# Performance work log

Hardware: AMD Instinct MI355X
Metric: run time of the kernel (lower is better)

## Reference

```python
import jax, jax.numpy as jnp
import numpy as np

T = 2048          # tokens
HID = 4096        # hidden_size
H = 32            # n_heads
D = 192           # head_dim
DR = 64           # qk_rope_head_dim
Q_LORA = 1536
O_LORA = 512
G = 4             # o_groups
EPS = 1e-6
MAX_POS = 4096
ROPE_BASE = 10000.0
SCALE = D ** -0.5


def _rmsnorm(x, weight=None, eps=EPS):
    # normalize over last dim in fp32, like the triton kernel / RMSNorm
    xf = x.astype(jnp.float32)
    rms_inv = jax.lax.rsqrt(jnp.mean(xf * xf, axis=-1, keepdims=True) + eps)
    out = xf * rms_inv
    if weight is not None:
        out = out * weight
    return out.astype(x.dtype)


def _apply_rope(x, cos, sin):
    # x: [..., DR]; interleaved complex rotation (deepseek-style freqs_cis mult)
    x2 = x.reshape(x.shape[:-1] + (DR // 2, 2))
    a, b = x2[..., 0], x2[..., 1]
    ra = a * cos - b * sin
    rb = a * sin + b * cos
    return jnp.stack([ra, rb], axis=-1).reshape(x.shape)


def setup_inputs() -> dict:
    key = jax.random.key(0)
    ks = jax.random.split(key, 12)
    s = lambda k, shape, scale: jax.random.normal(k, shape, dtype=jnp.float32) * scale
    x = s(ks[0], (T, HID), 1.0)
    positions = jnp.arange(T, dtype=jnp.int64)
    wq_a = s(ks[1], (Q_LORA, HID), HID ** -0.5)
    q_norm_w = jnp.ones((Q_LORA,), jnp.float32)
    wq_b = s(ks[2], (H * D, Q_LORA), Q_LORA ** -0.5)
    wkv = s(ks[3], (D, HID), HID ** -0.5)
    kv_norm_w = jnp.ones((D,), jnp.float32)
    attn_sink = s(ks[4], (H,), 1.0)
    wo_a = s(ks[5], (G * O_LORA, (H * D) // G), ((H * D) // G) ** -0.5)
    wo_b = s(ks[6], (HID, G * O_LORA), (G * O_LORA) ** -0.5)
    # precomputed rope tables [MAX_POS, DR//2]
    inv_freq = 1.0 / (ROPE_BASE ** (np.arange(0, DR, 2, dtype=np.float32) / DR))
    t = np.arange(MAX_POS, dtype=np.float32)
    freqs = np.outer(t, inv_freq)
    rope_cos = jnp.asarray(np.cos(freqs))
    rope_sin = jnp.asarray(np.sin(freqs))
    return dict(x=x, positions=positions, wq_a=wq_a, q_norm_w=q_norm_w, wq_b=wq_b,
                wkv=wkv, kv_norm_w=kv_norm_w, attn_sink=attn_sink, wo_a=wo_a,
                wo_b=wo_b, rope_cos=rope_cos, rope_sin=rope_sin)


def reference(x, positions, wq_a, q_norm_w, wq_b, wkv, kv_norm_w, attn_sink,
              wo_a, wo_b, rope_cos, rope_sin):
    cos = rope_cos[positions]  # [T, DR//2]
    sin = rope_sin[positions]

    # q path: wq_a -> RMSNorm(weighted) -> wq_b -> per-head unweighted RMSNorm -> RoPE
    q_lora = _rmsnorm(x @ wq_a.T, q_norm_w)                # [T, Q_LORA]
    q = (q_lora @ wq_b.T).reshape(T, H, D)                 # [T, H, D]
    q = _rmsnorm(q)                                        # per-head rms_normalize
    q_rope = _apply_rope(q[..., -DR:], cos[:, None, :], sin[:, None, :])
    q = jnp.concatenate([q[..., :-DR], q_rope], axis=-1)

    # shared single kv head: wkv -> kv_norm -> RoPE on rope dims
    kv = _rmsnorm(x @ wkv.T, kv_norm_w)                    # [T, D]
    kv_rope = _apply_rope(kv[..., -DR:], cos, sin)
    kv = jnp.concatenate([kv[..., :-DR], kv_rope], axis=-1)

    # MQA attention with attention sink and causal mask
    scores = jnp.einsum('thd,sd->ths', q, kv).astype(jnp.float32) * SCALE  # [T,H,S]
    causal = positions[:, None] >= positions[None, :]       # [T, S]
    scores = jnp.where(causal[:, None, :], scores, -jnp.inf)
    sink = jnp.broadcast_to(attn_sink[None, :, None], (T, H, 1))
    logits = jnp.concatenate([scores, sink], axis=-1)       # [T, H, S+1]
    probs = jax.nn.softmax(logits, axis=-1)[..., :-1]       # drop sink column
    out = jnp.einsum('ths,sd->thd', probs.astype(kv.dtype), kv)  # [T, H, D]

    # grouped low-rank output projection: wo_a per group, then wo_b
    out_g = out.reshape(T, G, (H * D) // G)
    wo_a_g = wo_a.reshape(G, O_LORA, (H * D) // G)
    o_low = jnp.einsum('tgi,goi->tgo', out_g, wo_a_g).reshape(T, G * O_LORA)
    y = o_low @ wo_b.T                                      # [T, HID]
    return y
```

## Files before the change

kernel.cpp:

```cpp
#include <hip/hip_runtime.h>
#include <hip/hip_bf16.h>

#define T_TOK 2048
#define HIDN  4096
#define NH    32
#define HD    192
#define QLORA 1536
#define OLORA 512
#define NG    4
#define NFUSE 1728

typedef unsigned short u16;
typedef __attribute__((ext_vector_type(8))) short short8;
typedef __attribute__((ext_vector_type(4))) short short4v;
typedef __attribute__((ext_vector_type(4))) float f32x4;

__device__ __forceinline__ float b2f(u16 u) {
  union { unsigned int u; float f; } x; x.u = ((unsigned int)u) << 16; return x.f;
}
__device__ __forceinline__ u16 f2b(float f) {
  union { float f; unsigned int u; } x; x.f = f;
  unsigned int r = x.u + 0x7fff + ((x.u >> 16) & 1);
  return (u16)(r >> 16);
}

#define GLOAD16(gp, lp) __builtin_amdgcn_global_load_lds( \
    (const __attribute__((address_space(1))) unsigned int*)(gp), \
    (__attribute__((address_space(3))) unsigned int*)(lp), 16, 0, 0)
#define SCHEDB() __builtin_amdgcn_sched_barrier(0)
#define SBAR()   __builtin_amdgcn_s_barrier()

__global__ __launch_bounds__(256) void cast_f32_bf16(const float* __restrict__ src,
                                                     u16* __restrict__ dst, long n4) {
  long i = (long)blockIdx.x * blockDim.x + threadIdx.x;
  long stride = (long)gridDim.x * blockDim.x;
  for (long j = i; j < n4; j += stride) {
    float4 v = *reinterpret_cast<const float4*>(src + j * 4);
    short4v o;
    o[0] = (short)f2b(v.x); o[1] = (short)f2b(v.y);
    o[2] = (short)f2b(v.z); o[3] = (short)f2b(v.w);
    *reinterpret_cast<short4v*>(dst + j * 4) = o;
  }
}

template <int OM>
__global__ __launch_bounds__(256)
void gemm_bt(const u16* __restrict__ A, const u16* __restrict__ B,
             void* __restrict__ Cout, int M, int N, int K,
             int lda, int ldb, int ldc,
             long a_goff, long b_goff, long c_goff) {
  A += (long)blockIdx.z * a_goff;
  B += (long)blockIdx.z * b_goff;
  __shared__ u16 As[2][128 * 32];
  __shared__ u16 Bs[2][128 * 32];
  const int tid = threadIdx.x;
  const int lane = tid & 63;
  const int wave = tid >> 6;
  const int lg = lane >> 4, lr = lane & 15;
  const int wm = (wave >> 1) * 64, wn = (wave & 1) * 64;
  const int m0 = blockIdx.x * 128, n0 = blockIdx.y * 128;

  const int i0 = tid, i1 = tid + 256;
  const int ra0 = i0 >> 2, ka0 = (i0 & 3) * 8;
  const int ra1 = i1 >> 2, ka1 = (i1 & 3) * 8;
  const u16* pA0 = A + (long)(m0 + ra0) * lda + ka0;
  const u16* pA1 = A + (long)(m0 + ra1) * lda + ka1;
  int rb0 = n0 + ra0; if (rb0 > N - 1) rb0 = N - 1;
  int rb1 = n0 + ra1; if (rb1 > N - 1) rb1 = N - 1;
  const u16* pB0 = B + (long)rb0 * ldb + ka0;
  const u16* pB1 = B + (long)rb1 * ldb + ka1;
  const int woff = wave * 1024;

  f32x4 acc[4][4];
#pragma unroll
  for (int a = 0; a < 4; a++)
#pragma unroll
    for (int b = 0; b < 4; b++) acc[a][b] = f32x4{0.f, 0.f, 0.f, 0.f};

  GLOAD16(pA0, (char*)As + woff);
  GLOAD16(pA1, (char*)As + 4096 + woff);
  GLOAD16(pB0, (char*)Bs + woff);
  GLOAD16(pB1, (char*)Bs + 4096 + woff);

  const int nk = K >> 5;
  int buf = 0;
  for (int kk = 0; kk < nk; ++kk) {
    const int kn = (kk + 1 < nk) ? (kk + 1) * 32 : kk * 32;
    {
      char* dA = (char*)As + (buf ^ 1) * 8192 + woff;
      char* dB = (char*)Bs + (buf ^ 1) * 8192 + woff;
      GLOAD16(pA0 + kn, dA);
      GLOAD16(pA1 + kn, dA + 4096);
      GLOAD16(pB0 + kn, dB);
      GLOAD16(pB1 + kn, dB + 4096);
    }
    asm volatile("s_waitcnt vmcnt(4)" ::: "memory");
    SCHEDB(); SBAR(); SCHEDB();

    short8 af[4], bf[4];
#pragma unroll
    for (int i = 0; i < 4; i++)
      af[i] = *reinterpret_cast<const short8*>(&As[buf][(wm + i * 16 + lr) * 32 + lg * 8]);
#pragma unroll
    for (int i = 0; i < 4; i++)
      bf[i] = *reinterpret_cast<const short8*>(&Bs[buf][(wn + i * 16 + lr) * 32 + lg * 8]);
#pragma unroll
    for (int mi = 0; mi < 4; mi++)
#pragma unroll
      for (int ni = 0; ni < 4; ni++)
        acc[mi][ni] = __builtin_amdgcn_mfma_f32_16x16x32_bf16(af[mi], bf[ni], acc[mi][ni], 0, 0, 0);

    SCHEDB(); SBAR(); SCHEDB();
    buf ^= 1;
  }
  asm volatile("s_waitcnt vmcnt(0)" ::: "memory");

  const long cbase = (long)blockIdx.z * c_goff;
#pragma unroll
  for (int mi = 0; mi < 4; mi++) {
#pragma unroll
    for (int ni = 0; ni < 4; ni++) {
      int col = n0 + wn + ni * 16 + lr;
      if (col < N) {
#pragma unroll
        for (int i = 0; i < 4; i++) {
          int row = m0 + wm + mi * 16 + lg * 4 + i;
          float v = acc[mi][ni][i];
          if constexpr (OM == 0)
            reinterpret_cast<u16*>(Cout)[cbase + (long)row * ldc + col] = f2b(v);
          else
            reinterpret_cast<float*>(Cout)[cbase + (long)row * ldc + col] = v;
        }
      }
    }
  }
}

__global__ __launch_bounds__(256)
void rmsnorm_rows(u16* __restrict__ buf, const float* __restrict__ w) {
  const int row = blockIdx.x;
  u16* p = buf + (long)row * NFUSE;
  const int tid = threadIdx.x;
  float v[6];
  float ss = 0.f;
#pragma unroll
  for (int j = 0; j < 6; j++) { v[j] = b2f(p[tid + j * 256]); ss += v[j] * v[j]; }
#pragma unroll
  for (int m = 1; m < 64; m <<= 1) ss += __shfl_xor(ss, m);
  __shared__ float red[4];
  if ((tid & 63) == 0) red[tid >> 6] = ss;
  __syncthreads();
  ss = red[0] + red[1] + red[2] + red[3];
  float rinv = rsqrtf(ss * (1.0f / QLORA) + 1e-6f);
#pragma unroll
  for (int j = 0; j < 6; j++) p[tid + j * 256] = f2b(v[j] * rinv * w[tid + j * 256]);
}

__global__ __launch_bounds__(256)
void qnorm_rope(u16* __restrict__ q, const int* __restrict__ pos,
                const float* __restrict__ rc, const float* __restrict__ rs) {
  const int t = blockIdx.x, h = blockIdx.y * 4 + (threadIdx.x >> 6);
  u16* p = q + (long)t * (NH * HD) + h * HD;
  const int lane = threadIdx.x & 63;
  float v0 = b2f(p[lane]), v1 = b2f(p[lane + 64]), v2 = b2f(p[lane + 128]);
  float ss = v0 * v0 + v1 * v1 + v2 * v2;
#pragma unroll
  for (int m = 1; m < 64; m <<= 1) ss += __shfl_xor(ss, m);
  float rinv = rsqrtf(ss * (1.0f / HD) + 1e-6f);
  v0 *= rinv; v1 *= rinv; v2 *= rinv;
  float partner = __shfl_xor(v2, 1);
  int pp = pos[t];
  int j = lane >> 1;
  float c = rc[pp * 32 + j], s = rs[pp * 32 + j];
  float r = ((lane & 1) == 0) ? (v2 * c - partner * s) : (partner * s + v2 * c);
  p[lane] = f2b(v0); p[lane + 64] = f2b(v1); p[lane + 128] = f2b(r);
}

__global__ __launch_bounds__(256)
void kvnorm_rope(const u16* __restrict__ t1f, u16* __restrict__ kvb,
                 u16* __restrict__ kvT, const float* __restrict__ w,
                 const int* __restrict__ pos,
                 const float* __restrict__ rc, const float* __restrict__ rs) {
  const int t = blockIdx.x * 4 + (threadIdx.x >> 6);
  const u16* src = t1f + (long)t * NFUSE + QLORA;
  u16* p = kvb + (long)t * HD;
  const int lane = threadIdx.x & 63;
  float v0 = b2f(src[lane]), v1 = b2f(src[lane + 64]), v2 = b2f(src[lane + 128]);
  float ss = v0 * v0 + v1 * v1 + v2 * v2;
#pragma unroll
  for (int m = 1; m < 64; m <<= 1) ss += __shfl_xor(ss, m);
  float rinv = rsqrtf(ss * (1.0f / HD) + 1e-6f);
  v0 *= rinv * w[lane]; v1 *= rinv * w[lane + 64]; v2 *= rinv * w[lane + 128];
  float partner = __shfl_xor(v2, 1);
  int pp = pos[t];
  int j = lane >> 1;
  float c = rc[pp * 32 + j], s = rs[pp * 32 + j];
  float r = ((lane & 1) == 0) ? (v2 * c - partner * s) : (partner * s + v2 * c);
  u16 o0 = f2b(v0), o1 = f2b(v1), o2 = f2b(r);
  p[lane] = o0; p[lane + 64] = o1; p[lane + 128] = o2;
  kvT[(long)lane * T_TOK + t] = o0;
  kvT[(long)(lane + 64) * T_TOK + t] = o1;
  kvT[(long)(lane + 128) * T_TOK + t] = o2;
}

__global__ __launch_bounds__(512)
void attn(const u16* __restrict__ q, const u16* __restrict__ kv,
          const u16* __restrict__ kvT, const float* __restrict__ sink,
          u16* __restrict__ out) {
  __shared__ u16 Ks[2][64 * 192];
  __shared__ u16 Vs[2][192 * 64];
  __shared__ u16 P[8][16 * 68];
  const int tid = threadIdx.x;
  const int wave = tid >> 6, lane = tid & 63;
  const int lg = lane >> 4, lr = lane & 15;
  const int h = blockIdx.y * 8 + wave;
  u16* Pw = P[wave];

  int krow[3], koff[3], vrow[3], voff[3];
#pragma unroll
  for (int j = 0; j < 3; j++) {
    int s = tid + j * 512;
    int rk = s / 24, ck = s - rk * 24;
    krow[j] = rk; koff[j] = (ck ^ (rk & 7)) * 8;
    int rv = s >> 3, cv = s & 7;
    vrow[j] = rv; voff[j] = (cv ^ (rv & 7)) * 8;
  }
  const float sk = sink[h];
  const float scale = 0.07216878364870323f;
  int buf = 0;

  for (int pass = 0; pass < 2; ++pass) {
    const int qb = pass ? blockIdx.x : (127 - blockIdx.x);
    const int q0 = qb * 16;
    const int s_end = q0 + 16;
    const int nt = (s_end + 63) >> 6;

    short8 qf[6];
#pragma unroll
    for (int c = 0; c < 6; c++)
      qf[c] = *reinterpret_cast<const short8*>(
          q + (long)(q0 + lr) * (NH * HD) + h * HD + c * 32 + lg * 8);

    f32x4 acc[12];
#pragma unroll
    for (int c = 0; c < 12; c++) acc[c] = f32x4{0.f, 0.f, 0.f, 0.f};
    float mr[4], lrow[4];
#pragma unroll
    for (int i = 0; i < 4; i++) { mr[i] = sk; lrow[i] = 1.0f; }

    {
      char* dK = (char*)Ks[buf]; char* dV = (char*)Vs[buf];
#pragma unroll
      for (int j = 0; j < 3; j++)
        GLOAD16(kv + (long)krow[j] * HD + koff[j], dK + (tid + j * 512) * 16);
#pragma unroll
      for (int j = 0; j < 3; j++)
        GLOAD16(kvT + (long)vrow[j] * T_TOK + voff[j], dV + (tid + j * 512) * 16);
    }

    for (int t = 0; t < nt; ++t) {
      const int s0 = t * 64;
      const int sn = (t + 1 < nt) ? s0 + 64 : s0;
      {
        char* dK = (char*)Ks[buf ^ 1]; char* dV = (char*)Vs[buf ^ 1];
#pragma unroll
        for (int j = 0; j < 3; j++)
          GLOAD16(kv + (long)(sn + krow[j]) * HD + koff[j], dK + (tid + j * 512) * 16);
#pragma unroll
        for (int j = 0; j < 3; j++)
          GLOAD16(kvT + (long)vrow[j] * T_TOK + sn + voff[j], dV + (tid + j * 512) * 16);
      }
      asm volatile("s_waitcnt vmcnt(6)" ::: "memory");
      SCHEDB(); SBAR(); SCHEDB();

      const u16* Kb = Ks[buf];
      const u16* Vb = Vs[buf];
      f32x4 sc[4];
      __builtin_amdgcn_s_setprio(1);
#pragma unroll
      for (int sub = 0; sub < 4; sub++) {
        int c0 = s0 + sub * 16;
        f32x4 v = f32x4{0.f, 0.f, 0.f, 0.f};
        if (c0 < s_end) {
#pragma unroll
          for (int c = 0; c < 6; c++) {
            short8 kf = *reinterpret_cast<const short8*>(
                &Kb[((sub * 16 + lr) * HD + c * 32 + lg * 8) ^ ((lr & 7) << 3)]);
            v = __builtin_amdgcn_mfma_f32_16x16x32_bf16(qf[c], kf, v, 0, 0, 0);
          }
          int scol = c0 + lr;
#pragma unroll
          for (int i = 0; i < 4; i++) {
            int qrow = q0 + lg * 4 + i;
            v[i] = (scol <= qrow) ? v[i] * scale : -__builtin_inff();
          }
        } else {
#pragma unroll
          for (int i = 0; i < 4; i++) v[i] = -__builtin_inff();
        }
        sc[sub] = v;
      }
      __builtin_amdgcn_s_setprio(0);

      float mn[4];
#pragma unroll
      for (int i = 0; i < 4; i++) {
        float tm = fmaxf(fmaxf(sc[0][i], sc[1][i]), fmaxf(sc[2][i], sc[3][i]));
#pragma unroll
        for (int m = 1; m < 16; m <<= 1) tm = fmaxf(tm, __shfl_xor(tm, m));
        mn[i] = fmaxf(mr[i], tm);
      }
      bool need = (mn[0] > mr[0]) | (mn[1] > mr[1]) | (mn[2] > mr[2]) | (mn[3] > mr[3]);
      if (__any(need)) {
#pragma unroll
        for (int i = 0; i < 4; i++) {
          float f = __expf(mr[i] - mn[i]);
          lrow[i] *= f; mr[i] = mn[i];
#pragma unroll
          for (int c = 0; c < 12; c++) acc[c][i] *= f;
        }
      }
      float pr[4][4];
#pragma unroll
      for (int i = 0; i < 4; i++) {
        float rsum = 0.f;
#pragma unroll
        for (int sub = 0; sub < 4; sub++) { pr[sub][i] = __expf(sc[sub][i] - mr[i]); rsum += pr[sub][i]; }
#pragma unroll
        for (int m = 1; m < 16; m <<= 1) rsum += __shfl_xor(rsum, m);
        lrow[i] += rsum;
      }
#pragma unroll
      for (int sub = 0; sub < 4; sub++)
#pragma unroll
        for (int i = 0; i < 4; i++)
          Pw[(lg * 4 + i) * 68 + sub * 16 + lr] = f2b(pr[sub][i]);
      short8 pf0 = *reinterpret_cast<const short8*>(&Pw[lr * 68 + lg * 8]);
      short8 pf1 = *reinterpret_cast<const short8*>(&Pw[lr * 68 + 32 + lg * 8]);

      __builtin_amdgcn_s_setprio(1);
#pragma unroll
      for (int c = 0; c < 12; c++) {
        short8 vf = *reinterpret_cast<const short8*>(
            &Vb[((c * 16 + lr) * 64 + lg * 8) ^ ((lr & 7) << 3)]);
        acc[c] = __builtin_amdgcn_mfma_f32_16x16x32_bf16(pf0, vf, acc[c], 0, 0, 0);
      }
      if (s0 + 32 < s_end) {
#pragma unroll
        for (int c = 0; c < 12; c++) {
          short8 vf = *reinterpret_cast<const short8*>(
              &Vb[((c * 16 + lr) * 64 + 32 + lg * 8) ^ ((lr & 7) << 3)]);
          acc[c] = __builtin_amdgcn_mfma_f32_16x16x32_bf16(pf1, vf, acc[c], 0, 0, 0);
        }
      }
      __builtin_amdgcn_s_setprio(0);

      SCHEDB(); SBAR(); SCHEDB();
      buf ^= 1;
    }

    asm volatile("s_waitcnt vmcnt(0)" ::: "memory");
#pragma unroll
    for (int c = 0; c < 12; c++)
#pragma unroll
      for (int i = 0; i < 4; i++) {
        int qrow = q0 + lg * 4 + i;
        out[(long)qrow * (NH * HD) + h * HD + c * 16 + lr] = f2b(acc[c][i] / lrow[i]);
      }
    SBAR();
  }
}

extern "C" void kernel_launch(void* const* d_in, const int* in_sizes, int n_in,
                              void* d_out, int out_size, void* d_ws, size_t ws_size,
                              hipStream_t stream) {
  const float* x    = (const float*)d_in[0];
  const int* pos    = (const int*)d_in[1];
  const float* wq_a = (const float*)d_in[2];
  const float* q_nw = (const float*)d_in[3];
  const float* wq_b = (const float*)d_in[4];
  const float* wkv  = (const float*)d_in[5];
  const float* kvnw = (const float*)d_in[6];
  const float* sink = (const float*)d_in[7];
  const float* wo_a = (const float*)d_in[8];
  const float* wo_b = (const float*)d_in[9];
  const float* rcos = (const float*)d_in[10];
  const float* rsin = (const float*)d_in[11];
  float* y = (float*)d_out;

  char* ws = (char*)d_ws;
  size_t off = 0;
  auto alloc = [&](size_t bytes) -> void* {
    void* p = ws + off;
    off += (bytes + 255) & ~(size_t)255;
    return p;
  };
  u16* xb   = (u16*)alloc((size_t)T_TOK * HIDN * 2);
  u16* wqab = (u16*)alloc((size_t)QLORA * HIDN * 2);
  u16* wkvb = (u16*)alloc((size_t)HD * HIDN * 2);
  u16* wqbb = (u16*)alloc((size_t)NH * HD * QLORA * 2);
  u16* woab = (u16*)alloc((size_t)NG * OLORA * 1536 * 2);
  u16* wobb = (u16*)alloc((size_t)HIDN * NG * OLORA * 2);
  u16* t1f  = (u16*)alloc((size_t)T_TOK * NFUSE * 2);
  u16* qn   = (u16*)alloc((size_t)T_TOK * NH * HD * 2);
  u16* kvb  = (u16*)alloc((size_t)T_TOK * HD * 2);
  u16* kvT  = (u16*)alloc((size_t)HD * T_TOK * 2);
  u16* ao   = (u16*)alloc((size_t)T_TOK * NH * HD * 2);
  u16* olow = (u16*)alloc((size_t)T_TOK * NG * OLORA * 2);

  auto cast = [&](const float* s, u16* d, long n) {
    long n4 = n / 4;
    long blocks = (n4 + 255) / 256;
    if (blocks > 2048) blocks = 2048;
    hipLaunchKernelGGL(cast_f32_bf16, dim3((int)blocks), dim3(256), 0, stream, s, d, n4);
  };
  cast(x, xb, (long)T_TOK * HIDN);
  cast(wq_a, wqab, (long)QLORA * HIDN);
  cast(wkv, wkvb, (long)HD * HIDN);
  cast(wq_b, wqbb, (long)NH * HD * QLORA);
  cast(wo_a, woab, (long)NG * OLORA * 1536);
  cast(wo_b, wobb, (long)HIDN * NG * OLORA);

  hipLaunchKernelGGL((gemm_bt<0>), dim3(16, 14, 1), dim3(256), 0, stream,
                     xb, wqab, (void*)t1f, 2048, NFUSE, 4096, 4096, 4096, NFUSE, 0L, 0L, 0L);
  hipLaunchKernelGGL(rmsnorm_rows, dim3(2048), dim3(256), 0, stream, t1f, q_nw);
  hipLaunchKernelGGL(kvnorm_rope, dim3(512), dim3(256), 0, stream,
                     t1f, kvb, kvT, kvnw, pos, rcos, rsin);
  hipLaunchKernelGGL((gemm_bt<0>), dim3(16, 48, 1), dim3(256), 0, stream,
                     t1f, wqbb, (void*)qn, 2048, 6144, 1536, NFUSE, 1536, 6144, 0L, 0L, 0L);
  hipLaunchKernelGGL(qnorm_rope, dim3(2048, 8), dim3(256), 0, stream, qn, pos, rcos, rsin);
  hipLaunchKernelGGL(attn, dim3(64, 4), dim3(512), 0, stream, qn, kvb, kvT, sink, ao);
  hipLaunchKernelGGL((gemm_bt<0>), dim3(16, 4, 4), dim3(256), 0, stream,
                     ao, woab, (void*)olow, 2048, 512, 1536, 6144, 1536, 2048,
                     1536L, (long)512 * 1536, 512L);
  hipLaunchKernelGGL((gemm_bt<1>), dim3(16, 32, 1), dim3(256), 0, stream,
                     olow, wobb, (void*)y, 2048, 4096, 2048, 2048, 2048, 4096, 0L, 0L, 0L);
}
```

Measured before the change: 410.3 us.

## Stage attention K/V through registers, single LDS buffer, fold scale into Q for exp2

The attention kernel moves from 512-thread blocks with double-buffered async global-to-LDS copies to 256-thread blocks (4 heads each, grid doubled) with a single LDS buffer. The next K/V tile is prefetched into registers and written to LDS after compute, behind an extra barrier. The softmax scale times log2(e) is folded into Q during qnorm_rope, so the kernel uses exp2f and drops the per-score multiply. This halves LDS per block, which may allow more resident blocks, at the cost of more registers and an extra barrier per tile, plus a bf16 rounding change from pre-scaling Q.

```diff
diff --git a/kernel.cpp b/kernel.cpp
--- a/kernel.cpp
+++ b/kernel.cpp
@@ -162,6 +162,7 @@
   const int t = blockIdx.x, h = blockIdx.y * 4 + (threadIdx.x >> 6);
   u16* p = q + (long)t * (NH * HD) + h * HD;
   const int lane = threadIdx.x & 63;
+  const float QS = 0.07216878364870323f * 1.4426950408889634f;
   float v0 = b2f(p[lane]), v1 = b2f(p[lane + 64]), v2 = b2f(p[lane + 128]);
   float ss = v0 * v0 + v1 * v1 + v2 * v2;
 #pragma unroll
@@ -173,7 +174,7 @@
   int j = lane >> 1;
   float c = rc[pp * 32 + j], s = rs[pp * 32 + j];
   float r = ((lane & 1) == 0) ? (v2 * c - partner * s) : (partner * s + v2 * c);
-  p[lane] = f2b(v0); p[lane + 64] = f2b(v1); p[lane + 128] = f2b(r);
+  p[lane] = f2b(v0 * QS); p[lane + 64] = f2b(v1 * QS); p[lane + 128] = f2b(r * QS);
 }
 
 __global__ __launch_bounds__(256)
@@ -203,34 +204,55 @@
   kvT[(long)(lane + 128) * T_TOK + t] = o2;
 }
 
-__global__ __launch_bounds__(512)
+__global__ __launch_bounds__(256)
 void attn(const u16* __restrict__ q, const u16* __restrict__ kv,
           const u16* __restrict__ kvT, const float* __restrict__ sink,
           u16* __restrict__ out) {
-  __shared__ u16 Ks[2][64 * 192];
-  __shared__ u16 Vs[2][192 * 64];
-  __shared__ u16 P[8][16 * 68];
+  __shared__ u16 Ks[64 * 192];
+  __shared__ u16 Vs[192 * 64];
+  __shared__ u16 P[4][16 * 68];
   const int tid = threadIdx.x;
   const int wave = tid >> 6, lane = tid & 63;
   const int lg = lane >> 4, lr = lane & 15;
-  const int h = blockIdx.y * 8 + wave;
+  const int h = blockIdx.y * 4 + wave;
   u16* Pw = P[wave];
 
-  int krow[3], koff[3], vrow[3], voff[3];
-#pragma unroll
-  for (int j = 0; j < 3; j++) {
-    int s = tid + j * 512;
+  int krow[6], kcol[6], klds[6], vrow[6], vcol[6], vlds[6];
+#pragma unroll
+  for (int j = 0; j < 6; j++) {
+    int s = tid + j * 256;
     int rk = s / 24, ck = s - rk * 24;
-    krow[j] = rk; koff[j] = (ck ^ (rk & 7)) * 8;
+    krow[j] = rk; kcol[j] = ck * 8;
+    klds[j] = (rk * 24 + (ck ^ (rk & 7))) * 16;
     int rv = s >> 3, cv = s & 7;
-    vrow[j] = rv; voff[j] = (cv ^ (rv & 7)) * 8;
+    vrow[j] = rv; vcol[j] = cv * 8;
+    vlds[j] = (rv * 8 + (cv ^ (rv & 7))) * 16;
   }
-  const float sk = sink[h];
-  const float scale = 0.07216878364870323f;
-  int buf = 0;
+  const float sk = sink[h] * 1.4426950408889634f;
+
+  short8 kst[6], vst[6];
+#define STAGE_LOAD(SN) do { \
+    _Pragma("unroll") \
+    for (int j = 0; j < 6; j++) \
+      kst[j] = *reinterpret_cast<const short8*>(kv + (long)((SN) + krow[j]) * HD + kcol[j]); \
+    _Pragma("unroll") \
+    for (int j = 0; j < 6; j++) \
+      vst[j] = *reinterpret_cast<const short8*>(kvT + (long)vrow[j] * T_TOK + (SN) + vcol[j]); \
+  } while (0)
+#define STAGE_WRITE() do { \
+    _Pragma("unroll") \
+    for (int j = 0; j < 6; j++) \
+      *reinterpret_cast<short8*>((char*)Ks + klds[j]) = kst[j]; \
+    _Pragma("unroll") \
+    for (int j = 0; j < 6; j++) \
+      *reinterpret_cast<short8*>((char*)Vs + vlds[j]) = vst[j]; \
+  } while (0)
+
+  STAGE_LOAD(0);
+  SCHEDB();
 
   for (int pass = 0; pass < 2; ++pass) {
-    const int qb = pass ? blockIdx.x : (127 - blockIdx.x);
+    const int qb = pass ? (int)blockIdx.x : (127 - (int)blockIdx.x);
     const int q0 = qb * 16;
     const int s_end = q0 + 16;
     const int nt = (s_end + 63) >> 6;
@@ -248,33 +270,18 @@
 #pragma unroll
     for (int i = 0; i < 4; i++) { mr[i] = sk; lrow[i] = 1.0f; }
 
-    {
-      char* dK = (char*)Ks[buf]; char* dV = (char*)Vs[buf];
-#pragma unroll
-      for (int j = 0; j < 3; j++)
-        GLOAD16(kv + (long)krow[j] * HD + koff[j], dK + (tid + j * 512) * 16);
-#pragma unroll
-      for (int j = 0; j < 3; j++)
-        GLOAD16(kvT + (long)vrow[j] * T_TOK + voff[j], dV + (tid + j * 512) * 16);
-    }
+    asm volatile("s_waitcnt vmcnt(6)" ::: "memory");
+    SCHEDB();
+    STAGE_WRITE();
+    asm volatile("s_waitcnt lgkmcnt(0)" ::: "memory");
+    SCHEDB(); SBAR(); SCHEDB();
 
     for (int t = 0; t < nt; ++t) {
       const int s0 = t * 64;
-      const int sn = (t + 1 < nt) ? s0 + 64 : s0;
-      {
-        char* dK = (char*)Ks[buf ^ 1]; char* dV = (char*)Vs[buf ^ 1];
-#pragma unroll
-        for (int j = 0; j < 3; j++)
-          GLOAD16(kv + (long)(sn + krow[j]) * HD + koff[j], dK + (tid + j * 512) * 16);
-#pragma unroll
-        for (int j = 0; j < 3; j++)
-          GLOAD16(kvT + (long)vrow[j] * T_TOK + sn + voff[j], dV + (tid + j * 512) * 16);
-      }
-      asm volatile("s_waitcnt vmcnt(6)" ::: "memory");
-      SCHEDB(); SBAR(); SCHEDB();
-
-      const u16* Kb = Ks[buf];
-      const u16* Vb = Vs[buf];
+      if (t + 1 < nt) STAGE_LOAD(s0 + 64);
+      else if (pass == 0) STAGE_LOAD(0);
+      SCHEDB();
+
       f32x4 sc[4];
       __builtin_amdgcn_s_setprio(1);
 #pragma unroll
@@ -285,14 +292,14 @@
 #pragma unroll
           for (int c = 0; c < 6; c++) {
             short8 kf = *reinterpret_cast<const short8*>(
-                &Kb[((sub * 16 + lr) * HD + c * 32 + lg * 8) ^ ((lr & 7) << 3)]);
+                &Ks[((sub * 16 + lr) * HD + c * 32 + lg * 8) ^ ((lr & 7) << 3)]);
             v = __builtin_amdgcn_mfma_f32_16x16x32_bf16(qf[c], kf, v, 0, 0, 0);
           }
           int scol = c0 + lr;
 #pragma unroll
           for (int i = 0; i < 4; i++) {
             int qrow = q0 + lg * 4 + i;
-            v[i] = (scol <= qrow) ? v[i] * scale : -__builtin_inff();
+            v[i] = (scol <= qrow) ? v[i] : -__builtin_inff();
           }
         } else {
 #pragma unroll
@@ -314,7 +321,7 @@
       if (__any(need)) {
 #pragma unroll
         for (int i = 0; i < 4; i++) {
-          float f = __expf(mr[i] - mn[i]);
+          float f = exp2f(mr[i] - mn[i]);
           lrow[i] *= f; mr[i] = mn[i];
 #pragma unroll
           for (int c = 0; c < 12; c++) acc[c][i] *= f;
@@ -325,7 +332,7 @@
       for (int i = 0; i < 4; i++) {
         float rsum = 0.f;
 #pragma unroll
-        for (int sub = 0; sub < 4; sub++) { pr[sub][i] = __expf(sc[sub][i] - mr[i]); rsum += pr[sub][i]; }
+        for (int sub = 0; sub < 4; sub++) { pr[sub][i] = exp2f(sc[sub][i] - mr[i]); rsum += pr[sub][i]; }
 #pragma unroll
         for (int m = 1; m < 16; m <<= 1) rsum += __shfl_xor(rsum, m);
         lrow[i] += rsum;
@@ -342,24 +349,29 @@
 #pragma unroll
       for (int c = 0; c < 12; c++) {
         short8 vf = *reinterpret_cast<const short8*>(
-            &Vb[((c * 16 + lr) * 64 + lg * 8) ^ ((lr & 7) << 3)]);
+            &Vs[((c * 16 + lr) * 64 + lg * 8) ^ ((lr & 7) << 3)]);
         acc[c] = __builtin_amdgcn_mfma_f32_16x16x32_bf16(pf0, vf, acc[c], 0, 0, 0);
       }
       if (s0 + 32 < s_end) {
 #pragma unroll
         for (int c = 0; c < 12; c++) {
           short8 vf = *reinterpret_cast<const short8*>(
-              &Vb[((c * 16 + lr) * 64 + 32 + lg * 8) ^ ((lr & 7) << 3)]);
+              &Vs[((c * 16 + lr) * 64 + 32 + lg * 8) ^ ((lr & 7) << 3)]);
           acc[c] = __builtin_amdgcn_mfma_f32_16x16x32_bf16(pf1, vf, acc[c], 0, 0, 0);
         }
       }
       __builtin_amdgcn_s_setprio(0);
 
       SCHEDB(); SBAR(); SCHEDB();
-      buf ^= 1;
+      if (t + 1 < nt) {
+        asm volatile("s_waitcnt vmcnt(0)" ::: "memory");
+        SCHEDB();
+        STAGE_WRITE();
+        asm volatile("s_waitcnt lgkmcnt(0)" ::: "memory");
+      }
+      SCHEDB(); SBAR(); SCHEDB();
     }
 
-    asm volatile("s_waitcnt vmcnt(0)" ::: "memory");
 #pragma unroll
     for (int c = 0; c < 12; c++)
 #pragma unroll
@@ -367,8 +379,9 @@
         int qrow = q0 + lg * 4 + i;
         out[(long)qrow * (NH * HD) + h * HD + c * 16 + lr] = f2b(acc[c][i] / lrow[i]);
       }
-    SBAR();
   }
+#undef STAGE_LOAD
+#undef STAGE_WRITE
 }
 
 extern "C" void kernel_launch(void* const* d_in, const int* in_sizes, int n_in,
@@ -429,7 +442,7 @@
   hipLaunchKernelGGL((gemm_bt<0>), dim3(16, 48, 1), dim3(256), 0, stream,
                      t1f, wqbb, (void*)qn, 2048, 6144, 1536, NFUSE, 1536, 6144, 0L, 0L, 0L);
   hipLaunchKernelGGL(qnorm_rope, dim3(2048, 8), dim3(256), 0, stream, qn, pos, rcos, rsin);
-  hipLaunchKernelGGL(attn, dim3(64, 4), dim3(512), 0, stream, qn, kvb, kvT, sink, ao);
+  hipLaunchKernelGGL(attn, dim3(64, 8), dim3(256), 0, stream, qn, kvb, kvT, sink, ao);
   hipLaunchKernelGGL((gemm_bt<0>), dim3(16, 4, 4), dim3(256), 0, stream,
                      ao, woab, (void*)olow, 2048, 512, 1536, 6144, 1536, 2048,
                      1536L, (long)512 * 1536, 512L);
```

Result: slower. 570.0 us (+38.9%).

## Process both causal query blocks in one shared KV pass, fold scale into q

Applied to the files above, without the earlier changes.

The attention kernel now walks the KV tiles once and feeds each loaded tile to both the long and the short query block, which were handled in two separate passes before. This removes the duplicate loads of the shared prefix for the short block. The softmax scale and log2(e) are folded into q in the qnorm kernel so the attention loop can use exp2f and skip the per-score multiply. Launch bounds now request 2 blocks per SM, but the kernel holds two sets of accumulators and Q fragments, which raises register pressure and risks spills. Storing a pre-scaled q in bf16 also shifts rounding slightly.

```diff
diff --git a/kernel.cpp b/kernel.cpp
--- a/kernel.cpp
+++ b/kernel.cpp
@@ -162,6 +162,7 @@
   const int t = blockIdx.x, h = blockIdx.y * 4 + (threadIdx.x >> 6);
   u16* p = q + (long)t * (NH * HD) + h * HD;
   const int lane = threadIdx.x & 63;
+  const float QS = 0.07216878364870323f * 1.4426950408889634f;
   float v0 = b2f(p[lane]), v1 = b2f(p[lane + 64]), v2 = b2f(p[lane + 128]);
   float ss = v0 * v0 + v1 * v1 + v2 * v2;
 #pragma unroll
@@ -173,7 +174,7 @@
   int j = lane >> 1;
   float c = rc[pp * 32 + j], s = rs[pp * 32 + j];
   float r = ((lane & 1) == 0) ? (v2 * c - partner * s) : (partner * s + v2 * c);
-  p[lane] = f2b(v0); p[lane + 64] = f2b(v1); p[lane + 128] = f2b(r);
+  p[lane] = f2b(v0 * QS); p[lane + 64] = f2b(v1 * QS); p[lane + 128] = f2b(r * QS);
 }
 
 __global__ __launch_bounds__(256)
@@ -203,18 +204,21 @@
   kvT[(long)(lane + 128) * T_TOK + t] = o2;
 }
 
-__global__ __launch_bounds__(512)
+__global__ __launch_bounds__(512, 2)
 void attn(const u16* __restrict__ q, const u16* __restrict__ kv,
           const u16* __restrict__ kvT, const float* __restrict__ sink,
           u16* __restrict__ out) {
   __shared__ u16 Ks[2][64 * 192];
   __shared__ u16 Vs[2][192 * 64];
-  __shared__ u16 P[8][16 * 68];
+  __shared__ u16 P[8][2][16 * 68];
   const int tid = threadIdx.x;
   const int wave = tid >> 6, lane = tid & 63;
   const int lg = lane >> 4, lr = lane & 15;
   const int h = blockIdx.y * 8 + wave;
-  u16* Pw = P[wave];
+  const int bx = blockIdx.x;
+  const int q0L = (127 - bx) * 16, q0S = bx * 16;
+  const int s_endL = q0L + 16, s_endS = q0S + 16;
+  const int ntL = (s_endL + 63) >> 6;
 
   int krow[3], koff[3], vrow[3], voff[3];
 #pragma unroll
@@ -225,56 +229,55 @@
     int rv = s >> 3, cv = s & 7;
     vrow[j] = rv; voff[j] = (cv ^ (rv & 7)) * 8;
   }
-  const float sk = sink[h];
-  const float scale = 0.07216878364870323f;
+  const float sk = sink[h] * 1.4426950408889634f;
+
+  short8 qfL[6], qfS[6];
+#pragma unroll
+  for (int c = 0; c < 6; c++) {
+    qfL[c] = *reinterpret_cast<const short8*>(
+        q + (long)(q0L + lr) * (NH * HD) + h * HD + c * 32 + lg * 8);
+    qfS[c] = *reinterpret_cast<const short8*>(
+        q + (long)(q0S + lr) * (NH * HD) + h * HD + c * 32 + lg * 8);
+  }
+
+  f32x4 accL[12], accS[12];
+#pragma unroll
+  for (int c = 0; c < 12; c++) { accL[c] = f32x4{0.f,0.f,0.f,0.f}; accS[c] = f32x4{0.f,0.f,0.f,0.f}; }
+  float mrL[4], lrL[4], mrS[4], lrS[4];
+#pragma unroll
+  for (int i = 0; i < 4; i++) { mrL[i] = sk; lrL[i] = 1.0f; mrS[i] = sk; lrS[i] = 1.0f; }
+
+  {
+    char* dK = (char*)Ks[0]; char* dV = (char*)Vs[0];
+#pragma unroll
+    for (int j = 0; j < 3; j++)
+      GLOAD16(kv + (long)krow[j] * HD + koff[j], dK + (tid + j * 512) * 16);
+#pragma unroll
+    for (int j = 0; j < 3; j++)
+      GLOAD16(kvT + (long)vrow[j] * T_TOK + voff[j], dV + (tid + j * 512) * 16);
+  }
+
   int buf = 0;
-
-  for (int pass = 0; pass < 2; ++pass) {
-    const int qb = pass ? blockIdx.x : (127 - blockIdx.x);
-    const int q0 = qb * 16;
-    const int s_end = q0 + 16;
-    const int nt = (s_end + 63) >> 6;
-
-    short8 qf[6];
-#pragma unroll
-    for (int c = 0; c < 6; c++)
-      qf[c] = *reinterpret_cast<const short8*>(
-          q + (long)(q0 + lr) * (NH * HD) + h * HD + c * 32 + lg * 8);
-
-    f32x4 acc[12];
-#pragma unroll
-    for (int c = 0; c < 12; c++) acc[c] = f32x4{0.f, 0.f, 0.f, 0.f};
-    float mr[4], lrow[4];
-#pragma unroll
-    for (int i = 0; i < 4; i++) { mr[i] = sk; lrow[i] = 1.0f; }
-
+  for (int t = 0; t < ntL; ++t) {
+    const int s0 = t * 64;
+    const int sn = (t + 1 < ntL) ? s0 + 64 : s0;
     {
-      char* dK = (char*)Ks[buf]; char* dV = (char*)Vs[buf];
+      char* dK = (char*)Ks[buf ^ 1]; char* dV = (char*)Vs[buf ^ 1];
 #pragma unroll
       for (int j = 0; j < 3; j++)
-        GLOAD16(kv + (long)krow[j] * HD + koff[j], dK + (tid + j * 512) * 16);
+        GLOAD16(kv + (long)(sn + krow[j]) * HD + koff[j], dK + (tid + j * 512) * 16);
 #pragma unroll
       for (int j = 0; j < 3; j++)
-        GLOAD16(kvT + (long)vrow[j] * T_TOK + voff[j], dV + (tid + j * 512) * 16);
+        GLOAD16(kvT + (long)vrow[j] * T_TOK + sn + voff[j], dV + (tid + j * 512) * 16);
     }
-
-    for (int t = 0; t < nt; ++t) {
-      const int s0 = t * 64;
-      const int sn = (t + 1 < nt) ? s0 + 64 : s0;
-      {
-        char* dK = (char*)Ks[buf ^ 1]; char* dV = (char*)Vs[buf ^ 1];
-#pragma unroll
-        for (int j = 0; j < 3; j++)
-          GLOAD16(kv + (long)(sn + krow[j]) * HD + koff[j], dK + (tid + j * 512) * 16);
-#pragma unroll
-        for (int j = 0; j < 3; j++)
-          GLOAD16(kvT + (long)vrow[j] * T_TOK + sn + voff[j], dV + (tid + j * 512) * 16);
-      }
-      asm volatile("s_waitcnt vmcnt(6)" ::: "memory");
-      SCHEDB(); SBAR(); SCHEDB();
-
-      const u16* Kb = Ks[buf];
-      const u16* Vb = Vs[buf];
+    asm volatile("s_waitcnt vmcnt(6)" ::: "memory");
+    SCHEDB(); SBAR(); SCHEDB();
+
+    const u16* Kb = Ks[buf];
+    const u16* Vb = Vs[buf];
+
+    auto process = [&](int q0, int s_end, const short8* qf, f32x4* acc,
+                       float* mr, float* lrow, u16* Pw) {
       f32x4 sc[4];
       __builtin_amdgcn_s_setprio(1);
 #pragma unroll
@@ -292,7 +295,7 @@
 #pragma unroll
           for (int i = 0; i < 4; i++) {
             int qrow = q0 + lg * 4 + i;
-            v[i] = (scol <= qrow) ? v[i] * scale : -__builtin_inff();
+            v[i] = (scol <= qrow) ? v[i] : -__builtin_inff();
           }
         } else {
 #pragma unroll
@@ -314,7 +317,7 @@
       if (__any(need)) {
 #pragma unroll
         for (int i = 0; i < 4; i++) {
-          float f = __expf(mr[i] - mn[i]);
+          float f = exp2f(mr[i] - mn[i]);
           lrow[i] *= f; mr[i] = mn[i];
 #pragma unroll
           for (int c = 0; c < 12; c++) acc[c][i] *= f;
@@ -325,7 +328,7 @@
       for (int i = 0; i < 4; i++) {
         float rsum = 0.f;
 #pragma unroll
-        for (int sub = 0; sub < 4; sub++) { pr[sub][i] = __expf(sc[sub][i] - mr[i]); rsum += pr[sub][i]; }
+        for (int sub = 0; sub < 4; sub++) { pr[sub][i] = exp2f(sc[sub][i] - mr[i]); rsum += pr[sub][i]; }
 #pragma unroll
         for (int m = 1; m < 16; m <<= 1) rsum += __shfl_xor(rsum, m);
         lrow[i] += rsum;
@@ -354,21 +357,26 @@
         }
       }
       __builtin_amdgcn_s_setprio(0);
-
-      SCHEDB(); SBAR(); SCHEDB();
-      buf ^= 1;
+    };
+
+    process(q0L, s_endL, qfL, accL, mrL, lrL, P[wave][0]);
+    if (s0 < s_endS)
+      process(q0S, s_endS, qfS, accS, mrS, lrS, P[wave][1]);
+
+    SCHEDB(); SBAR(); SCHEDB();
+    buf ^= 1;
+  }
+  asm volatile("s_waitcnt vmcnt(0)" ::: "memory");
+
+#pragma unroll
+  for (int c = 0; c < 12; c++)
+#pragma unroll
+    for (int i = 0; i < 4; i++) {
+      int qrowL = q0L + lg * 4 + i;
+      int qrowS = q0S + lg * 4 + i;
+      out[(long)qrowL * (NH * HD) + h * HD + c * 16 + lr] = f2b(accL[c][i] / lrL[i]);
+      out[(long)qrowS * (NH * HD) + h * HD + c * 16 + lr] = f2b(accS[c][i] / lrS[i]);
     }
-
-    asm volatile("s_waitcnt vmcnt(0)" ::: "memory");
-#pragma unroll
-    for (int c = 0; c < 12; c++)
-#pragma unroll
-      for (int i = 0; i < 4; i++) {
-        int qrow = q0 + lg * 4 + i;
-        out[(long)qrow * (NH * HD) + h * HD + c * 16 + lr] = f2b(acc[c][i] / lrow[i]);
-      }
-    SBAR();
-  }
 }
 
 extern "C" void kernel_launch(void* const* d_in, const int* in_sizes, int n_in,
```

Measured after the change: 556.7 us. +35.7%, slower.
